# Performance work log

Measured on AMD Instinct MI355X. Metric: run time of the kernel, lower is better.

## Reference

```python
import jax, jax.numpy as jnp
import numpy as np

N_NODES = 50000
N_EDGES = 800000
IN_C, HID_C, OUT_C = 128, 128, 64


def setup_inputs() -> dict:
    key = jax.random.key(0)
    ks = jax.random.split(key, 8)
    sc_in = 1.0 / np.sqrt(IN_C)
    sc_hid = 1.0 / np.sqrt(HID_C)
    return {
        "x": jax.random.normal(ks[0], (N_NODES, IN_C), dtype=jnp.float32),
        "edge_index": jax.random.randint(ks[1], (2, N_EDGES), 0, N_NODES, dtype=jnp.int64),
        "W1_l": jax.random.normal(ks[2], (IN_C, HID_C), dtype=jnp.float32) * sc_in,
        "b1": jnp.zeros((HID_C,), dtype=jnp.float32),
        "W1_r": jax.random.normal(ks[3], (IN_C, HID_C), dtype=jnp.float32) * sc_in,
        "W2_l": jax.random.normal(ks[4], (HID_C, OUT_C), dtype=jnp.float32) * sc_hid,
        "b2": jnp.zeros((OUT_C,), dtype=jnp.float32),
        "W2_r": jax.random.normal(ks[5], (HID_C, OUT_C), dtype=jnp.float32) * sc_hid,
    }


def _sage_conv(x, src, dst, W_l, b, W_r, num_nodes):
    # gather neighbor features along edges: messages flow src -> dst
    msg = x[src]                                             # [E, C]
    agg = jax.ops.segment_sum(msg, dst, num_segments=num_nodes)
    cnt = jax.ops.segment_sum(jnp.ones((src.shape[0],), x.dtype), dst,
                              num_segments=num_nodes)
    mean = agg / jnp.maximum(cnt, 1.0)[:, None]              # mean aggregation
    # PyG SAGEConv: lin_l(aggregated) + lin_r(root); bias on lin_l only
    return mean @ W_l + b + x @ W_r


def reference(x, edge_index, W1_l, b1, W1_r, W2_l, b2, W2_r):
    src, dst = edge_index[0], edge_index[1]
    n = x.shape[0]
    h = jax.nn.relu(_sage_conv(x, src, dst, W1_l, b1, W1_r, n))
    # dropout(p=0.2) is identity at inference (training=False)
    return _sage_conv(h, src, dst, W2_l, b2, W2_r, n)
```

## Files before the change

kernel.cpp:

```cpp
#include <hip/hip_runtime.h>

#define N_NODES 50000
#define N_EDGES 800000
#define IN_C 128
#define HID_C 128
#define OUT_C 64

#define NBUCK 500
#define NODES_PER_BUCK 100
#define BCAP 2560
#define BA_CHUNK 8192
#define BA_BLOCKS ((N_EDGES + BA_CHUNK - 1) / BA_CHUNK)

#define XB_BLOCKS 6250
#define W1T_BLOCKS 128
#define W2T_BLOCKS 64
#define PREP_BLOCKS (XB_BLOCKS + W1T_BLOCKS + W2T_BLOCKS)
#define FUSED_BLOCKS (BA_BLOCKS + PREP_BLOCKS)

typedef __bf16 bf16x8 __attribute__((ext_vector_type(8)));
typedef __bf16 bf16x4 __attribute__((ext_vector_type(4)));
typedef float  f32x4  __attribute__((ext_vector_type(4)));

__global__ __launch_bounds__(256) void prep_bucketA_kernel(const float* __restrict__ x,
                                                           const float* __restrict__ W1l,
                                                           const float* __restrict__ W1r,
                                                           const float* __restrict__ W2l,
                                                           const float* __restrict__ W2r,
                                                           __bf16* __restrict__ xb,
                                                           __bf16* __restrict__ W1T,
                                                           __bf16* __restrict__ W2T,
                                                           const int* __restrict__ src,
                                                           const int* __restrict__ dst,
                                                           int* __restrict__ cursor,
                                                           unsigned* __restrict__ ebuf) {
    __shared__ int cnt[NBUCK];
    __shared__ int gbase[NBUCK];
    __shared__ int lcur[NBUCK];
    const int blk = blockIdx.x, t = threadIdx.x;
    if (blk < BA_BLOCKS) {
        for (int i = t; i < NBUCK; i += 256) cnt[i] = 0;
        __syncthreads();
        const int e0 = blk * BA_CHUNK;
        const int e1 = (e0 + BA_CHUNK < N_EDGES) ? e0 + BA_CHUNK : N_EDGES;
        for (int e = e0 + t; e < e1; e += 256)
            atomicAdd(&cnt[dst[e] / NODES_PER_BUCK], 1);
        __syncthreads();
        for (int i = t; i < NBUCK; i += 256) {
            gbase[i] = i * BCAP + atomicAdd(&cursor[i], cnt[i]);
            lcur[i] = 0;
        }
        __syncthreads();
        for (int e = e0 + t; e < e1; e += 256) {
            int d = dst[e];
            int b = d / NODES_PER_BUCK;
            int idx = gbase[b] + atomicAdd(&lcur[b], 1);
            if (idx < (b + 1) * BCAP)
                ebuf[idx] = (unsigned)src[e] | ((unsigned)(d - b * NODES_PER_BUCK) << 16);
        }
        return;
    }
    const int b = blk - BA_BLOCKS;
    if (b < XB_BLOCKS) {
        int i = b * 256 + t;
        float4 v = ((const float4*)x)[i];
        bf16x4 o = { (__bf16)v.x, (__bf16)v.y, (__bf16)v.z, (__bf16)v.w };
        ((bf16x4*)xb)[i] = o;
    } else if (b < XB_BLOCKS + W1T_BLOCKS) {
        int i = (b - XB_BLOCKS) * 256 + t;
        int n = i >> 8, kk = i & 255;
        float v = (kk < 128) ? W1l[kk * 128 + n] : W1r[(kk - 128) * 128 + n];
        W1T[i] = (__bf16)v;
    } else {
        int i = (b - XB_BLOCKS - W1T_BLOCKS) * 256 + t;
        int n = i >> 7, k = i & 127;
        float v = (n < 64) ? W2l[k * 64 + n] : W2r[k * 64 + (n - 64)];
        W2T[i] = (__bf16)v;
    }
}

__global__ __launch_bounds__(256) void bucketB_kernel(const unsigned* __restrict__ ebuf,
                                                      const int* __restrict__ cursor,
                                                      int* __restrict__ row_ptr,
                                                      int* __restrict__ srcs) {
    __shared__ int psum[256];
    __shared__ int deg[NODES_PER_BUCK];
    __shared__ int ofs[NODES_PER_BUCK + 1];
    const int b = blockIdx.x, t = threadIdx.x;
    int part = 0;
    for (int i = t; i < b; i += 256) {
        int c = cursor[i];
        if (c > BCAP) c = BCAP;
        part += c;
    }
    psum[t] = part;
    __syncthreads();
    for (int off = 128; off > 0; off >>= 1) {
        if (t < off) psum[t] += psum[t + off];
        __syncthreads();
    }
    const int rbase = psum[0];
    int m = cursor[b];
    if (m > BCAP) m = BCAP;
    const int node0 = b * NODES_PER_BUCK;
    const unsigned* eb = ebuf + (size_t)b * BCAP;

    for (int i = t; i < NODES_PER_BUCK; i += 256) deg[i] = 0;
    __syncthreads();
    for (int i = t; i < m; i += 256)
        atomicAdd(&deg[eb[i] >> 16], 1);
    __syncthreads();
    if (t == 0) {
        int s = 0;
        for (int i = 0; i < NODES_PER_BUCK; ++i) { ofs[i] = s; s += deg[i]; }
        ofs[NODES_PER_BUCK] = s;
    }
    __syncthreads();
    for (int i = t; i < NODES_PER_BUCK; i += 256) row_ptr[node0 + i] = rbase + ofs[i];
    if (b == 0 && t == 0) row_ptr[N_NODES] = N_EDGES;
    for (int i = t; i < NODES_PER_BUCK; i += 256) deg[i] = ofs[i];
    __syncthreads();
    for (int i = t; i < m; i += 256) {
        unsigned p = eb[i];
        int d = (int)(p >> 16);
        int pos = atomicAdd(&deg[d], 1);
        srcs[rbase + pos] = (int)(p & 0xFFFFu);
    }
}

__global__ __launch_bounds__(256) void agg_x_kernel(const __bf16* __restrict__ xb,
                                                    const int* __restrict__ row_ptr,
                                                    const int* __restrict__ srcs,
                                                    __bf16* __restrict__ m1) {
    const int wid = threadIdx.x >> 6, lane = threadIdx.x & 63;
    const int n = blockIdx.x * 4 + wid;
    if (n >= N_NODES) return;
    const int beg = row_ptr[n], end = row_ptr[n + 1];
    const int grp = lane >> 4;
    const int c   = lane & 15;
    float acc[8] = {};
    int s = beg + grp;
    for (; s + 12 < end; s += 16) {
        int u0 = srcs[s];
        int u1 = srcs[s + 4];
        int u2 = srcs[s + 8];
        int u3 = srcs[s + 12];
        bf16x8 v0 = *(const bf16x8*)(xb + (size_t)u0 * 128 + c * 8);
        bf16x8 v1 = *(const bf16x8*)(xb + (size_t)u1 * 128 + c * 8);
        bf16x8 v2 = *(const bf16x8*)(xb + (size_t)u2 * 128 + c * 8);
        bf16x8 v3 = *(const bf16x8*)(xb + (size_t)u3 * 128 + c * 8);
#pragma unroll
        for (int j = 0; j < 8; j++) acc[j] += (float)v0[j];
#pragma unroll
        for (int j = 0; j < 8; j++) acc[j] += (float)v1[j];
#pragma unroll
        for (int j = 0; j < 8; j++) acc[j] += (float)v2[j];
#pragma unroll
        for (int j = 0; j < 8; j++) acc[j] += (float)v3[j];
    }
    for (; s < end; s += 4) {
        int u = srcs[s];
        bf16x8 v = *(const bf16x8*)(xb + (size_t)u * 128 + c * 8);
#pragma unroll
        for (int j = 0; j < 8; j++) acc[j] += (float)v[j];
    }
#pragma unroll
    for (int j = 0; j < 8; j++) {
        acc[j] += __shfl_xor(acc[j], 16, 64);
        acc[j] += __shfl_xor(acc[j], 32, 64);
    }
    float cnt = (float)(end - beg);
    if (cnt < 1.f) cnt = 1.f;
    if (grp == 0) {
        bf16x8 o;
#pragma unroll
        for (int j = 0; j < 8; j++) o[j] = (__bf16)(acc[j] / cnt);
        *(bf16x8*)(m1 + (size_t)n * 128 + c * 8) = o;
    }
}

#define LDK 72
#define LDH 136

__global__ __launch_bounds__(256) void gemm12_kernel(const __bf16* __restrict__ A0,
                                                     const __bf16* __restrict__ A1,
                                                     const __bf16* __restrict__ W1T,
                                                     const __bf16* __restrict__ W2T,
                                                     const float* __restrict__ b1,
                                                     __bf16* __restrict__ Y,
                                                     float* __restrict__ Z, int M) {
    __shared__ __bf16 As[128 * LDH];
    __shared__ __bf16 Bs[128 * LDK];
    const int tid = threadIdx.x;
    const int row0 = blockIdx.x * 128;
    const int wave = tid >> 6, lane = tid & 63;
    const int wm = (wave & 1) * 64, wn = (wave >> 1) * 64;
    const int lr = lane & 15, quad = lane >> 4;

    f32x4 acc[4][4] = {};
    for (int ks = 0; ks < 256; ks += 64) {
        const __bf16* Asrc = (ks < 128) ? A0 : A1;
        const int kofs = (ks < 128) ? ks : ks - 128;
        for (int i = tid; i < 128 * 8; i += 256) {
            int r = i >> 3, ch = i & 7;
            int gr = row0 + r;
            float4 v = {0.f, 0.f, 0.f, 0.f};
            if (gr < M) v = *(const float4*)(Asrc + (size_t)gr * 128 + kofs + ch * 8);
            *(float4*)(As + r * LDH + ch * 8) = v;
        }
        for (int i = tid; i < 128 * 8; i += 256) {
            int r = i >> 3, ch = i & 7;
            float4 v = *(const float4*)(W1T + (size_t)r * 256 + ks + ch * 8);
            *(float4*)(Bs + r * LDK + ch * 8) = v;
        }
        __syncthreads();
#pragma unroll
        for (int k0 = 0; k0 < 64; k0 += 32) {
            bf16x8 af[4], bfr[4];
#pragma unroll
            for (int mt = 0; mt < 4; mt++)
                af[mt] = *(const bf16x8*)(As + (wm + mt * 16 + lr) * LDH + k0 + quad * 8);
#pragma unroll
            for (int nt = 0; nt < 4; nt++)
                bfr[nt] = *(const bf16x8*)(Bs + (wn + nt * 16 + lr) * LDK + k0 + quad * 8);
#pragma unroll
            for (int mt = 0; mt < 4; mt++)
#pragma unroll
                for (int nt = 0; nt < 4; nt++)
                    acc[mt][nt] = __builtin_amdgcn_mfma_f32_16x16x32_bf16(af[mt], bfr[nt], acc[mt][nt], 0, 0, 0);
        }
        __syncthreads();
    }

#pragma unroll
    for (int mt = 0; mt < 4; mt++) {
#pragma unroll
        for (int r = 0; r < 4; r++) {
            int row = wm + mt * 16 + quad * 4 + r;
#pragma unroll
            for (int nt = 0; nt < 4; nt++) {
                int col = wn + nt * 16 + lr;
                float v = acc[mt][nt][r] + b1[col];
                v = v > 0.f ? v : 0.f;
                As[row * LDH + col] = (__bf16)v;
            }
        }
    }

    f32x4 acc2[4][4] = {};
    for (int kh = 0; kh < 128; kh += 64) {
        for (int i = tid; i < 128 * 8; i += 256) {
            int r = i >> 3, ch = i & 7;
            float4 v = *(const float4*)(W2T + (size_t)r * 128 + kh + ch * 8);
            *(float4*)(Bs + r * LDK + ch * 8) = v;
        }
        __syncthreads();
#pragma unroll
        for (int k0 = 0; k0 < 64; k0 += 32) {
            bf16x8 af[4], bfr[4];
#pragma unroll
            for (int mt = 0; mt < 4; mt++)
                af[mt] = *(const bf16x8*)(As + (wm + mt * 16 + lr) * LDH + kh + k0 + quad * 8);
#pragma unroll
            for (int nt = 0; nt < 4; nt++)
                bfr[nt] = *(const bf16x8*)(Bs + (wn + nt * 16 + lr) * LDK + k0 + quad * 8);
#pragma unroll
            for (int mt = 0; mt < 4; mt++)
#pragma unroll
                for (int nt = 0; nt < 4; nt++)
                    acc2[mt][nt] = __builtin_amdgcn_mfma_f32_16x16x32_bf16(af[mt], bfr[nt], acc2[mt][nt], 0, 0, 0);
        }
        __syncthreads();
    }

#pragma unroll
    for (int mt = 0; mt < 4; mt++) {
#pragma unroll
        for (int r = 0; r < 4; r++) {
            int gr = row0 + wm + mt * 16 + quad * 4 + r;
            if (gr >= M) continue;
#pragma unroll
            for (int nt = 0; nt < 4; nt++) {
                int gc = wn + nt * 16 + lr;
                float v = acc2[mt][nt][r];
                if (gc < 64) Y[(size_t)gr * 64 + gc] = (__bf16)v;
                else         Z[(size_t)gr * 64 + (gc - 64)] = v;
            }
        }
    }
}

__global__ __launch_bounds__(256) void agg2_kernel(const __bf16* __restrict__ Y,
                                                   const float* __restrict__ Z,
                                                   const int* __restrict__ row_ptr,
                                                   const int* __restrict__ srcs,
                                                   const float* __restrict__ b2,
                                                   float* __restrict__ out) {
    const int wid = threadIdx.x >> 6, lane = threadIdx.x & 63;
    const int n = blockIdx.x * 4 + wid;
    if (n >= N_NODES) return;
    const int beg = row_ptr[n], end = row_ptr[n + 1];
    const int grp = lane >> 3;
    const int c   = lane & 7;
    float4 z0 = {0,0,0,0}, z1 = {0,0,0,0}, bb0 = {0,0,0,0}, bb1 = {0,0,0,0};
    if (grp == 0) {
        z0 = *(const float4*)(Z + (size_t)n * 64 + c * 8);
        z1 = *(const float4*)(Z + (size_t)n * 64 + c * 8 + 4);
        bb0 = *(const float4*)(b2 + c * 8);
        bb1 = *(const float4*)(b2 + c * 8 + 4);
    }
    float acc[8] = {};
    int s = beg + grp;
    for (; s + 8 < end; s += 16) {
        int u0 = srcs[s];
        int u1 = srcs[s + 8];
        bf16x8 v0 = *(const bf16x8*)(Y + (size_t)u0 * 64 + c * 8);
        bf16x8 v1 = *(const bf16x8*)(Y + (size_t)u1 * 64 + c * 8);
#pragma unroll
        for (int j = 0; j < 8; j++) acc[j] += (float)v0[j];
#pragma unroll
        for (int j = 0; j < 8; j++) acc[j] += (float)v1[j];
    }
    if (s < end) {
        int u = srcs[s];
        bf16x8 v = *(const bf16x8*)(Y + (size_t)u * 64 + c * 8);
#pragma unroll
        for (int j = 0; j < 8; j++) acc[j] += (float)v[j];
    }
#pragma unroll
    for (int j = 0; j < 8; j++) {
        acc[j] += __shfl_xor(acc[j], 8, 64);
        acc[j] += __shfl_xor(acc[j], 16, 64);
        acc[j] += __shfl_xor(acc[j], 32, 64);
    }
    float cnt = (float)(end - beg);
    if (cnt < 1.f) cnt = 1.f;
    if (grp == 0) {
        float inv = 1.f / cnt;
        float4 o0 = { acc[0] * inv + bb0.x + z0.x, acc[1] * inv + bb0.y + z0.y,
                      acc[2] * inv + bb0.z + z0.z, acc[3] * inv + bb0.w + z0.w };
        float4 o1 = { acc[4] * inv + bb1.x + z1.x, acc[5] * inv + bb1.y + z1.y,
                      acc[6] * inv + bb1.z + z1.z, acc[7] * inv + bb1.w + z1.w };
        *(float4*)(out + (size_t)n * 64 + c * 8) = o0;
        *(float4*)(out + (size_t)n * 64 + c * 8 + 4) = o1;
    }
}


extern "C" void kernel_launch(void* const* d_in, const int* in_sizes, int n_in,
                              void* d_out, int out_size, void* d_ws, size_t ws_size,
                              hipStream_t stream) {
    const float* x   = (const float*)d_in[0];
    const int*   ei  = (const int*)d_in[1];
    const float* W1l = (const float*)d_in[2];
    const float* b1  = (const float*)d_in[3];
    const float* W1r = (const float*)d_in[4];
    const float* W2l = (const float*)d_in[5];
    const float* b2  = (const float*)d_in[6];
    const float* W2r = (const float*)d_in[7];
    float* out = (float*)d_out;

    size_t need = 0;
    auto count = [&](size_t bytes) { need += (bytes + 255) & ~(size_t)255; };
    count((size_t)NBUCK * BCAP * 4);
    count((size_t)NBUCK * 4);
    count((size_t)(N_NODES + 1) * 4);
    count((size_t)N_EDGES * 4);
    count((size_t)N_NODES * 128 * 2);
    count((size_t)128 * 256 * 2);
    count((size_t)128 * 128 * 2);
    count((size_t)N_NODES * 128 * 2);
    count((size_t)N_NODES * 64 * 2);
    count((size_t)N_NODES * 64 * 4);
    if (ws_size < need) return;

    char* ws = (char*)d_ws;
    size_t off = 0;
    auto alloc = [&](size_t bytes) -> void* {
        void* p = ws + off;
        off += (bytes + 255) & ~(size_t)255;
        return p;
    };
    unsigned* ebuf  = (unsigned*)alloc((size_t)NBUCK * BCAP * 4);
    int*    cursor  = (int*)alloc((size_t)NBUCK * 4);
    int*    row_ptr = (int*)alloc((size_t)(N_NODES + 1) * 4);
    int*    srcs    = (int*)alloc((size_t)N_EDGES * 4);
    __bf16* xb      = (__bf16*)alloc((size_t)N_NODES * 128 * 2);
    __bf16* W1T     = (__bf16*)alloc((size_t)128 * 256 * 2);
    __bf16* W2T     = (__bf16*)alloc((size_t)128 * 128 * 2);
    __bf16* m1      = (__bf16*)alloc((size_t)N_NODES * 128 * 2);
    __bf16* Y       = (__bf16*)alloc((size_t)N_NODES * 64 * 2);
    float*  Z       = (float*)alloc((size_t)N_NODES * 64 * 4);

    const int* src = ei;
    const int* dst = ei + N_EDGES;

    hipMemsetAsync(cursor, 0, (size_t)NBUCK * 4, stream);
    prep_bucketA_kernel<<<FUSED_BLOCKS, 256, 0, stream>>>(x, W1l, W1r, W2l, W2r,
                                                          xb, W1T, W2T,
                                                          src, dst, cursor, ebuf);
    bucketB_kernel<<<NBUCK, 256, 0, stream>>>(ebuf, cursor, row_ptr, srcs);
    agg_x_kernel<<<(N_NODES + 3) / 4, 256, 0, stream>>>(xb, row_ptr, srcs, m1);
    gemm12_kernel<<<(N_NODES + 127) / 128, 256, 0, stream>>>(m1, xb, W1T, W2T, b1, Y, Z, N_NODES);
    agg2_kernel<<<(N_NODES + 3) / 4, 256, 0, stream>>>(Y, Z, row_ptr, srcs, b2, out);
}
```

Baseline: 198.8 us.

## Replace bucketed CSR build with global-atomic counting sort, restage GEMM in LDS

The bucket-based two-pass CSR construction is replaced by per-node degree counting with global atomics, a per-block prefix scan for row pointers, and a separate placement kernel that scatters sources through per-node atomic cursors. The x-to-bf16 conversion now handles 8 elements per thread. The fused GEMM loads the full 256-wide A tile into LDS once and reads weight fragments straight from global memory, dropping the per-k-step B staging and barriers. The changes aim to cut launch and bucket overhead and GEMM sync, at the cost of heavy global atomic contention, an extra kernel launch, and nondeterministic neighbor order within each row.

```diff
diff --git a/kernel.cpp b/kernel.cpp
--- a/kernel.cpp
+++ b/kernel.cpp
@@ -8,11 +8,12 @@
 
 #define NBUCK 500
 #define NODES_PER_BUCK 100
-#define BCAP 2560
-#define BA_CHUNK 8192
+#define BA_CHUNK 4096
 #define BA_BLOCKS ((N_EDGES + BA_CHUNK - 1) / BA_CHUNK)
-
-#define XB_BLOCKS 6250
+#define PL_CHUNK 2048
+#define PL_BLOCKS ((N_EDGES + PL_CHUNK - 1) / PL_CHUNK)
+
+#define XB_BLOCKS 3125
 #define W1T_BLOCKS 128
 #define W2T_BLOCKS 64
 #define PREP_BLOCKS (XB_BLOCKS + W1T_BLOCKS + W2T_BLOCKS)
@@ -22,50 +23,38 @@
 typedef __bf16 bf16x4 __attribute__((ext_vector_type(4)));
 typedef float  f32x4  __attribute__((ext_vector_type(4)));
 
-__global__ __launch_bounds__(256) void prep_bucketA_kernel(const float* __restrict__ x,
-                                                           const float* __restrict__ W1l,
-                                                           const float* __restrict__ W1r,
-                                                           const float* __restrict__ W2l,
-                                                           const float* __restrict__ W2r,
-                                                           __bf16* __restrict__ xb,
-                                                           __bf16* __restrict__ W1T,
-                                                           __bf16* __restrict__ W2T,
-                                                           const int* __restrict__ src,
-                                                           const int* __restrict__ dst,
-                                                           int* __restrict__ cursor,
-                                                           unsigned* __restrict__ ebuf) {
-    __shared__ int cnt[NBUCK];
-    __shared__ int gbase[NBUCK];
-    __shared__ int lcur[NBUCK];
+__global__ __launch_bounds__(256) void prep_count_kernel(const float* __restrict__ x,
+                                                         const float* __restrict__ W1l,
+                                                         const float* __restrict__ W1r,
+                                                         const float* __restrict__ W2l,
+                                                         const float* __restrict__ W2r,
+                                                         __bf16* __restrict__ xb,
+                                                         __bf16* __restrict__ W1T,
+                                                         __bf16* __restrict__ W2T,
+                                                         const int* __restrict__ dst,
+                                                         int* __restrict__ deg) {
     const int blk = blockIdx.x, t = threadIdx.x;
     if (blk < BA_BLOCKS) {
-        for (int i = t; i < NBUCK; i += 256) cnt[i] = 0;
-        __syncthreads();
         const int e0 = blk * BA_CHUNK;
-        const int e1 = (e0 + BA_CHUNK < N_EDGES) ? e0 + BA_CHUNK : N_EDGES;
-        for (int e = e0 + t; e < e1; e += 256)
-            atomicAdd(&cnt[dst[e] / NODES_PER_BUCK], 1);
-        __syncthreads();
-        for (int i = t; i < NBUCK; i += 256) {
-            gbase[i] = i * BCAP + atomicAdd(&cursor[i], cnt[i]);
-            lcur[i] = 0;
-        }
-        __syncthreads();
-        for (int e = e0 + t; e < e1; e += 256) {
-            int d = dst[e];
-            int b = d / NODES_PER_BUCK;
-            int idx = gbase[b] + atomicAdd(&lcur[b], 1);
-            if (idx < (b + 1) * BCAP)
-                ebuf[idx] = (unsigned)src[e] | ((unsigned)(d - b * NODES_PER_BUCK) << 16);
+        const int rem = N_EDGES - e0;
+        const int nE = rem < BA_CHUNK ? rem : BA_CHUNK;
+        for (int q = 4 * t; q + 3 < nE; q += 1024) {
+            int4 d4 = *(const int4*)(dst + e0 + q);
+            atomicAdd(&deg[d4.x], 1);
+            atomicAdd(&deg[d4.y], 1);
+            atomicAdd(&deg[d4.z], 1);
+            atomicAdd(&deg[d4.w], 1);
         }
         return;
     }
     const int b = blk - BA_BLOCKS;
     if (b < XB_BLOCKS) {
         int i = b * 256 + t;
-        float4 v = ((const float4*)x)[i];
-        bf16x4 o = { (__bf16)v.x, (__bf16)v.y, (__bf16)v.z, (__bf16)v.w };
-        ((bf16x4*)xb)[i] = o;
+        float4 v0 = ((const float4*)x)[2 * i];
+        float4 v1 = ((const float4*)x)[2 * i + 1];
+        bf16x8 o = { (__bf16)v0.x, (__bf16)v0.y, (__bf16)v0.z, (__bf16)v0.w,
+                     (__bf16)v1.x, (__bf16)v1.y, (__bf16)v1.z, (__bf16)v1.w };
+        ((bf16x8*)xb)[i] = o;
     } else if (b < XB_BLOCKS + W1T_BLOCKS) {
         int i = (b - XB_BLOCKS) * 256 + t;
         int n = i >> 8, kk = i & 255;
@@ -79,52 +68,51 @@
     }
 }
 
-__global__ __launch_bounds__(256) void bucketB_kernel(const unsigned* __restrict__ ebuf,
-                                                      const int* __restrict__ cursor,
+__global__ __launch_bounds__(256) void csr_ptr_kernel(const int* __restrict__ deg,
                                                       int* __restrict__ row_ptr,
-                                                      int* __restrict__ srcs) {
+                                                      int* __restrict__ cur) {
     __shared__ int psum[256];
-    __shared__ int deg[NODES_PER_BUCK];
+    __shared__ int sdeg[NODES_PER_BUCK];
     __shared__ int ofs[NODES_PER_BUCK + 1];
     const int b = blockIdx.x, t = threadIdx.x;
+    const int node0 = b * NODES_PER_BUCK;
     int part = 0;
-    for (int i = t; i < b; i += 256) {
-        int c = cursor[i];
-        if (c > BCAP) c = BCAP;
-        part += c;
-    }
+    for (int i = t; i < node0; i += 256) part += deg[i];
     psum[t] = part;
+    if (t < NODES_PER_BUCK) sdeg[t] = deg[node0 + t];
     __syncthreads();
     for (int off = 128; off > 0; off >>= 1) {
         if (t < off) psum[t] += psum[t + off];
         __syncthreads();
     }
     const int rbase = psum[0];
-    int m = cursor[b];
-    if (m > BCAP) m = BCAP;
-    const int node0 = b * NODES_PER_BUCK;
-    const unsigned* eb = ebuf + (size_t)b * BCAP;
-
-    for (int i = t; i < NODES_PER_BUCK; i += 256) deg[i] = 0;
-    __syncthreads();
-    for (int i = t; i < m; i += 256)
-        atomicAdd(&deg[eb[i] >> 16], 1);
-    __syncthreads();
     if (t == 0) {
         int s = 0;
-        for (int i = 0; i < NODES_PER_BUCK; ++i) { ofs[i] = s; s += deg[i]; }
+        for (int i = 0; i < NODES_PER_BUCK; ++i) { ofs[i] = s; s += sdeg[i]; }
         ofs[NODES_PER_BUCK] = s;
     }
     __syncthreads();
-    for (int i = t; i < NODES_PER_BUCK; i += 256) row_ptr[node0 + i] = rbase + ofs[i];
+    if (t < NODES_PER_BUCK) {
+        row_ptr[node0 + t] = rbase + ofs[t];
+        cur[node0 + t] = rbase + ofs[t];
+    }
     if (b == 0 && t == 0) row_ptr[N_NODES] = N_EDGES;
-    for (int i = t; i < NODES_PER_BUCK; i += 256) deg[i] = ofs[i];
-    __syncthreads();
-    for (int i = t; i < m; i += 256) {
-        unsigned p = eb[i];
-        int d = (int)(p >> 16);
-        int pos = atomicAdd(&deg[d], 1);
-        srcs[rbase + pos] = (int)(p & 0xFFFFu);
+}
+
+__global__ __launch_bounds__(256) void place_kernel(const int* __restrict__ src,
+                                                    const int* __restrict__ dst,
+                                                    int* __restrict__ cur,
+                                                    int* __restrict__ srcs) {
+    const int e0 = blockIdx.x * PL_CHUNK, t = threadIdx.x;
+    const int rem = N_EDGES - e0;
+    const int nE = rem < PL_CHUNK ? rem : PL_CHUNK;
+    for (int q = 4 * t; q + 3 < nE; q += 1024) {
+        int4 s4 = *(const int4*)(src + e0 + q);
+        int4 d4 = *(const int4*)(dst + e0 + q);
+        srcs[atomicAdd(&cur[d4.x], 1)] = s4.x;
+        srcs[atomicAdd(&cur[d4.y], 1)] = s4.y;
+        srcs[atomicAdd(&cur[d4.z], 1)] = s4.z;
+        srcs[atomicAdd(&cur[d4.w], 1)] = s4.w;
     }
 }
 
@@ -179,8 +167,7 @@
     }
 }
 
-#define LDK 72
-#define LDH 136
+#define LDH2 264
 
 __global__ __launch_bounds__(256) void gemm12_kernel(const __bf16* __restrict__ A0,
                                                      const __bf16* __restrict__ A1,
@@ -189,48 +176,43 @@
                                                      const float* __restrict__ b1,
                                                      __bf16* __restrict__ Y,
                                                      float* __restrict__ Z, int M) {
-    __shared__ __bf16 As[128 * LDH];
-    __shared__ __bf16 Bs[128 * LDK];
+    __shared__ __bf16 As[128 * LDH2];
     const int tid = threadIdx.x;
     const int row0 = blockIdx.x * 128;
     const int wave = tid >> 6, lane = tid & 63;
     const int wm = (wave & 1) * 64, wn = (wave >> 1) * 64;
     const int lr = lane & 15, quad = lane >> 4;
 
+    for (int i = tid; i < 128 * 32; i += 256) {
+        int r = i >> 5, ch = i & 31;
+        int gr = row0 + r;
+        float4 v = {0.f, 0.f, 0.f, 0.f};
+        if (gr < M) {
+            const __bf16* p = (ch < 16) ? (A0 + (size_t)gr * 128 + ch * 8)
+                                        : (A1 + (size_t)gr * 128 + (ch - 16) * 8);
+            v = *(const float4*)p;
+        }
+        *(float4*)(As + r * LDH2 + ch * 8) = v;
+    }
+    __syncthreads();
+
     f32x4 acc[4][4] = {};
-    for (int ks = 0; ks < 256; ks += 64) {
-        const __bf16* Asrc = (ks < 128) ? A0 : A1;
-        const int kofs = (ks < 128) ? ks : ks - 128;
-        for (int i = tid; i < 128 * 8; i += 256) {
-            int r = i >> 3, ch = i & 7;
-            int gr = row0 + r;
-            float4 v = {0.f, 0.f, 0.f, 0.f};
-            if (gr < M) v = *(const float4*)(Asrc + (size_t)gr * 128 + kofs + ch * 8);
-            *(float4*)(As + r * LDH + ch * 8) = v;
-        }
-        for (int i = tid; i < 128 * 8; i += 256) {
-            int r = i >> 3, ch = i & 7;
-            float4 v = *(const float4*)(W1T + (size_t)r * 256 + ks + ch * 8);
-            *(float4*)(Bs + r * LDK + ch * 8) = v;
-        }
-        __syncthreads();
-#pragma unroll
-        for (int k0 = 0; k0 < 64; k0 += 32) {
-            bf16x8 af[4], bfr[4];
-#pragma unroll
-            for (int mt = 0; mt < 4; mt++)
-                af[mt] = *(const bf16x8*)(As + (wm + mt * 16 + lr) * LDH + k0 + quad * 8);
+#pragma unroll 4
+    for (int k = 0; k < 256; k += 32) {
+        bf16x8 af[4], bfr[4];
+#pragma unroll
+        for (int mt = 0; mt < 4; mt++)
+            af[mt] = *(const bf16x8*)(As + (wm + mt * 16 + lr) * LDH2 + k + quad * 8);
+#pragma unroll
+        for (int nt = 0; nt < 4; nt++)
+            bfr[nt] = *(const bf16x8*)(W1T + (size_t)(wn + nt * 16 + lr) * 256 + k + quad * 8);
+#pragma unroll
+        for (int mt = 0; mt < 4; mt++)
 #pragma unroll
             for (int nt = 0; nt < 4; nt++)
-                bfr[nt] = *(const bf16x8*)(Bs + (wn + nt * 16 + lr) * LDK + k0 + quad * 8);
-#pragma unroll
-            for (int mt = 0; mt < 4; mt++)
-#pragma unroll
-                for (int nt = 0; nt < 4; nt++)
-                    acc[mt][nt] = __builtin_amdgcn_mfma_f32_16x16x32_bf16(af[mt], bfr[nt], acc[mt][nt], 0, 0, 0);
-        }
-        __syncthreads();
-    }
+                acc[mt][nt] = __builtin_amdgcn_mfma_f32_16x16x32_bf16(af[mt], bfr[nt], acc[mt][nt], 0, 0, 0);
+    }
+    __syncthreads();
 
 #pragma unroll
     for (int mt = 0; mt < 4; mt++) {
@@ -242,35 +224,27 @@
                 int col = wn + nt * 16 + lr;
                 float v = acc[mt][nt][r] + b1[col];
                 v = v > 0.f ? v : 0.f;
-                As[row * LDH + col] = (__bf16)v;
+                As[row * LDH2 + col] = (__bf16)v;
             }
         }
     }
+    __syncthreads();
 
     f32x4 acc2[4][4] = {};
-    for (int kh = 0; kh < 128; kh += 64) {
-        for (int i = tid; i < 128 * 8; i += 256) {
-            int r = i >> 3, ch = i & 7;
-            float4 v = *(const float4*)(W2T + (size_t)r * 128 + kh + ch * 8);
-            *(float4*)(Bs + r * LDK + ch * 8) = v;
-        }
-        __syncthreads();
-#pragma unroll
-        for (int k0 = 0; k0 < 64; k0 += 32) {
-            bf16x8 af[4], bfr[4];
-#pragma unroll
-            for (int mt = 0; mt < 4; mt++)
-                af[mt] = *(const bf16x8*)(As + (wm + mt * 16 + lr) * LDH + kh + k0 + quad * 8);
+#pragma unroll
+    for (int k = 0; k < 128; k += 32) {
+        bf16x8 af[4], bfr[4];
+#pragma unroll
+        for (int mt = 0; mt < 4; mt++)
+            af[mt] = *(const bf16x8*)(As + (wm + mt * 16 + lr) * LDH2 + k + quad * 8);
+#pragma unroll
+        for (int nt = 0; nt < 4; nt++)
+            bfr[nt] = *(const bf16x8*)(W2T + (size_t)(wn + nt * 16 + lr) * 128 + k + quad * 8);
+#pragma unroll
+        for (int mt = 0; mt < 4; mt++)
 #pragma unroll
             for (int nt = 0; nt < 4; nt++)
-                bfr[nt] = *(const bf16x8*)(Bs + (wn + nt * 16 + lr) * LDK + k0 + quad * 8);
-#pragma unroll
-            for (int mt = 0; mt < 4; mt++)
-#pragma unroll
-                for (int nt = 0; nt < 4; nt++)
-                    acc2[mt][nt] = __builtin_amdgcn_mfma_f32_16x16x32_bf16(af[mt], bfr[nt], acc2[mt][nt], 0, 0, 0);
-        }
-        __syncthreads();
+                acc2[mt][nt] = __builtin_amdgcn_mfma_f32_16x16x32_bf16(af[mt], bfr[nt], acc2[mt][nt], 0, 0, 0);
     }
 
 #pragma unroll
@@ -362,8 +336,8 @@
 
     size_t need = 0;
     auto count = [&](size_t bytes) { need += (bytes + 255) & ~(size_t)255; };
-    count((size_t)NBUCK * BCAP * 4);
-    count((size_t)NBUCK * 4);
+    count((size_t)N_NODES * 4);
+    count((size_t)N_NODES * 4);
     count((size_t)(N_NODES + 1) * 4);
     count((size_t)N_EDGES * 4);
     count((size_t)N_NODES * 128 * 2);
@@ -381,8 +355,8 @@
         off += (bytes + 255) & ~(size_t)255;
         return p;
     };
-    unsigned* ebuf  = (unsigned*)alloc((size_t)NBUCK * BCAP * 4);
-    int*    cursor  = (int*)alloc((size_t)NBUCK * 4);
+    int*    deg     = (int*)alloc((size_t)N_NODES * 4);
+    int*    cur     = (int*)alloc((size_t)N_NODES * 4);
     int*    row_ptr = (int*)alloc((size_t)(N_NODES + 1) * 4);
     int*    srcs    = (int*)alloc((size_t)N_EDGES * 4);
     __bf16* xb      = (__bf16*)alloc((size_t)N_NODES * 128 * 2);
@@ -395,11 +369,11 @@
     const int* src = ei;
     const int* dst = ei + N_EDGES;
 
-    hipMemsetAsync(cursor, 0, (size_t)NBUCK * 4, stream);
-    prep_bucketA_kernel<<<FUSED_BLOCKS, 256, 0, stream>>>(x, W1l, W1r, W2l, W2r,
-                                                          xb, W1T, W2T,
-                                                          src, dst, cursor, ebuf);
-    bucketB_kernel<<<NBUCK, 256, 0, stream>>>(ebuf, cursor, row_ptr, srcs);
+    hipMemsetAsync(deg, 0, (size_t)N_NODES * 4, stream);
+    prep_count_kernel<<<FUSED_BLOCKS, 256, 0, stream>>>(x, W1l, W1r, W2l, W2r,
+                                                        xb, W1T, W2T, dst, deg);
+    csr_ptr_kernel<<<NBUCK, 256, 0, stream>>>(deg, row_ptr, cur);
+    place_kernel<<<PL_BLOCKS, 256, 0, stream>>>(src, dst, cur, srcs);
     agg_x_kernel<<<(N_NODES + 3) / 4, 256, 0, stream>>>(xb, row_ptr, srcs, m1);
     gemm12_kernel<<<(N_NODES + 127) / 128, 256, 0, stream>>>(m1, xb, W1T, W2T, b1, Y, Z, N_NODES);
     agg2_kernel<<<(N_NODES + 3) / 4, 256, 0, stream>>>(Y, Z, row_ptr, srcs, b2, out);
```

New measurement: 266.4 us. +34.0%, slower.
